# Kernel tuning notes

Measured on AMD Instinct MI355X. Metric: run time of the kernel, lower is better.

## Reference

```python
import jax, jax.numpy as jnp
import numpy as np

IMG = 640
SCORE_THR = 0.1
IOU_THR = 0.5
MAX_DET = 200  # fixed upper bound on kept boxes per class (jit-static)
BBOX_STD = (0.1, 0.1, 0.2, 0.2)  # standard RetinaNet delta std


def _make_anchors():
    # Standard RetinaNet anchors: P3-P7, 3 ratios x 3 scales, xyxy format.
    strides = [8, 16, 32, 64, 128]
    sizes = [32, 64, 128, 256, 512]
    ratios = np.array([0.5, 1.0, 2.0])
    scales = np.array([2 ** 0, 2 ** (1.0 / 3.0), 2 ** (2.0 / 3.0)])
    out = []
    for stride, size in zip(strides, sizes):
        n = IMG // stride
        ws = (size * scales[None, :] * np.sqrt(1.0 / ratios)[:, None]).reshape(-1)
        hs = (size * scales[None, :] * np.sqrt(ratios)[:, None]).reshape(-1)
        c = (np.arange(n) + 0.5) * stride
        CX, CY = np.meshgrid(c, c)
        ctr = np.stack([CX.ravel(), CY.ravel()], -1)  # [n*n, 2]
        wh = np.stack([ws, hs], -1)  # [9, 2]
        boxes = np.concatenate([ctr[:, None, :] - 0.5 * wh[None],
                                ctr[:, None, :] + 0.5 * wh[None]], -1)  # [n*n, 9, 4]
        out.append(boxes.reshape(-1, 4))
    return np.concatenate(out, 0).astype(np.float32)  # [76725, 4]


def setup_inputs() -> dict:
    key = jax.random.key(0)
    k1, k2 = jax.random.split(key)
    A = 76725
    C = 80
    classification = jax.random.uniform(k1, (1, A, C), dtype=jnp.float32)
    regression = jax.random.normal(k2, (1, A, 4), dtype=jnp.float32)
    anchors = jnp.asarray(_make_anchors())  # [A, 4] xyxy
    return {"classification": classification, "regression": regression, "anchors": anchors}


def _decode_and_clip(anchors, reg):
    aw = anchors[:, 2] - anchors[:, 0]
    ah = anchors[:, 3] - anchors[:, 1]
    ax = anchors[:, 0] + 0.5 * aw
    ay = anchors[:, 1] + 0.5 * ah
    cx = ax + reg[:, 0] * BBOX_STD[0] * aw
    cy = ay + reg[:, 1] * BBOX_STD[1] * ah
    w = aw * jnp.exp(reg[:, 2] * BBOX_STD[2])
    h = ah * jnp.exp(reg[:, 3] * BBOX_STD[3])
    x1 = jnp.clip(cx - 0.5 * w, 0.0, IMG)  # trimBox2Image
    y1 = jnp.clip(cy - 0.5 * h, 0.0, IMG)
    x2 = jnp.clip(cx + 0.5 * w, 0.0, IMG)
    y2 = jnp.clip(cy + 0.5 * h, 0.0, IMG)
    return jnp.stack([x1, y1, x2, y2], -1)  # [A, 4]


def reference(classification, regression, anchors):
    cls = classification[0]  # [A, C]
    boxes = _decode_and_clip(anchors, regression[0])  # [A, 4]
    A = cls.shape[0]
    C = cls.shape[1]
    idx = jnp.arange(A)
    areas = (boxes[:, 2] - boxes[:, 0]) * (boxes[:, 3] - boxes[:, 1])

    def nms_one(scores):  # scores: [A] for one class
        s0 = jnp.where(scores > SCORE_THR, scores, -1.0)
        keep0 = jnp.zeros((A,), dtype=bool)

        def step(carry, _):
            s, keep = carry
            i = jnp.argmax(s)
            valid = s[i] > 0.0
            keep = keep.at[i].set(valid)
            b = boxes[i]
            ix1 = jnp.maximum(b[0], boxes[:, 0])
            iy1 = jnp.maximum(b[1], boxes[:, 1])
            ix2 = jnp.minimum(b[2], boxes[:, 2])
            iy2 = jnp.minimum(b[3], boxes[:, 3])
            inter = jnp.clip(ix2 - ix1, 0.0) * jnp.clip(iy2 - iy1, 0.0)
            ab = (b[2] - b[0]) * (b[3] - b[1])
            iou = inter / (ab + areas - inter)
            sup = valid & ((iou > IOU_THR) | (idx == i))
            s = jnp.where(sup, -1.0, s)
            return (s, keep), None

        (_, keep), _ = jax.lax.scan(step, (s0, keep0), None, length=MAX_DET)
        return keep

    keep = jax.vmap(nms_one)(cls.T)  # [C, A] bool, greedy NMS per class
    final_scores = jnp.where(keep, cls.T, 0.0)  # [C, A]
    final_labels = jnp.where(keep, jnp.arange(C, dtype=jnp.int32)[:, None], -1)  # [C, A]
    final_boxes = jnp.where(keep[..., None], boxes[None], 0.0)  # [C, A, 4]
    return final_scores, final_labels, final_boxes, keep
```

## Files before the change

kernel.cpp:

```cpp
#include <hip/hip_runtime.h>
#include <cstdint>
#include <cstddef>

#pragma clang fp contract(off)

#define A_N 76725
#define C_N 80
#define CA_N (A_N * 80)
#define MAXDET 200
#define CAP 4096
#define NBIN 16
#define BCAP 256
#define IMG_F 640.0f
#define THR0 0.975f
#define CNT_STRIDE 32
#define FILLB 2480

typedef unsigned long long u64;

__device__ __forceinline__ bool iou_gt(float b0, float b1, float b2, float b3, float ab,
                                       float x0, float x1, float x2, float x3, float xa) {
    float ix1 = fmaxf(b0, x0);
    float iy1 = fmaxf(b1, x1);
    float ix2 = fminf(b2, x2);
    float iy2 = fminf(b3, x3);
    float iw = fmaxf(ix2 - ix1, 0.0f);
    float ih = fmaxf(iy2 - iy1, 0.0f);
    float inter = iw * ih;
    float den = ab + xa - inter;
    float iou = inter / den;
    return iou > 0.5f;
}

__device__ __forceinline__ float band_lo(int b) {
    return 0.975f - 0.025f * (float)b;
}

__global__ __launch_bounds__(256) void k_prep(const float* __restrict__ cls,
                                              const float* __restrict__ reg,
                                              const float* __restrict__ anc,
                                              float* __restrict__ boxes,
                                              int* __restrict__ gcnt,
                                              u64* __restrict__ gkeys) {
    int i = blockIdx.x * 256 + threadIdx.x;
    if (i < A_N) {
        float a0 = anc[i * 4 + 0], a1 = anc[i * 4 + 1];
        float a2 = anc[i * 4 + 2], a3 = anc[i * 4 + 3];
        float aw = a2 - a0;
        float ah = a3 - a1;
        float ax = a0 + 0.5f * aw;
        float ay = a1 + 0.5f * ah;
        float r0 = reg[i * 4 + 0], r1 = reg[i * 4 + 1];
        float r2 = reg[i * 4 + 2], r3 = reg[i * 4 + 3];
        float cx = ax + r0 * 0.1f * aw;
        float cy = ay + r1 * 0.1f * ah;
        float w = aw * expf(r2 * 0.2f);
        float h = ah * expf(r3 * 0.2f);
        float x1 = fminf(fmaxf(cx - 0.5f * w, 0.0f), IMG_F);
        float y1 = fminf(fmaxf(cy - 0.5f * h, 0.0f), IMG_F);
        float x2 = fminf(fmaxf(cx + 0.5f * w, 0.0f), IMG_F);
        float y2 = fminf(fmaxf(cy + 0.5f * h, 0.0f), IMG_F);
        boxes[i * 4 + 0] = x1;
        boxes[i * 4 + 1] = y1;
        boxes[i * 4 + 2] = x2;
        boxes[i * 4 + 3] = y2;
    }
    if (i < CA_N) {
        float s = cls[i];
        if (s > THR0) {
            int c = i % C_N;
            unsigned a = (unsigned)(i / C_N);
            int b = (int)((s - THR0) * 640.0f);
            b = b < 0 ? 0 : (b > (NBIN - 1) ? (NBIN - 1) : b);
            int slot = atomicAdd(&gcnt[(c * NBIN + b) * CNT_STRIDE], 1);
            if (slot < BCAP)
                gkeys[((size_t)(c * NBIN + b) << 8) + slot] =
                    ((u64)__float_as_uint(s) << 32) | (u64)(0xFFFFFFFFu - a);
        }
    }
}

__device__ __forceinline__ int resolve_run(const u64* seg, int cnt, int kept,
                                           const float4* __restrict__ boxes4,
                                           float4* kboxS, float* karea,
                                           int* kIdxL, float* kScrL,
                                           float4* cbxS, float* car,
                                           unsigned int* mlo, unsigned int* mhi,
                                           unsigned char* supp, int* keptL,
                                           int tid, int lane) {
    for (int cs = 0; cs < cnt && kept < MAXDET; cs += 64) {
        int nc = (cnt - cs < 64) ? (cnt - cs) : 64;
        float4 rb = make_float4(0.f, 0.f, 0.f, 0.f);
        float rar = 0.f, rsc = 0.f;
        int rix = 0;
        if (tid < 64) {
            mlo[tid] = 0;
            mhi[tid] = 0;
            supp[tid] = (tid < nc) ? 0 : 1;
            if (tid < nc) {
                u64 key = seg[cs + tid];
                rix = (int)(0xFFFFFFFFu - (unsigned)(key & 0xFFFFFFFFull));
                rsc = __uint_as_float((unsigned)(key >> 32));
                rb = boxes4[rix];
                rar = (rb.z - rb.x) * (rb.w - rb.y);
                cbxS[tid] = rb;
                car[tid] = rar;
            }
        }
        __syncthreads();

        {
            int i = tid >> 4, jl = tid & 15;
            if (i < nc) {
                float4 x = cbxS[i];
                float xa = car[i];
                bool s = false;
                for (int j = jl; j < kept; j += 16) {
                    float4 kb = kboxS[j];
                    if (iou_gt(kb.x, kb.y, kb.z, kb.w, karea[j],
                               x.x, x.y, x.z, x.w, xa)) { s = true; break; }
                }
                if (s) supp[i] = 1;
            }
        }
        {
            int i = tid & 63, jb = tid >> 6;
            if (i < nc) {
                float4 b = cbxS[i];
                float ba = car[i];
                unsigned int l32 = 0, h32 = 0;
                for (int j = jb; j < nc; j += 16) {
                    if (j > i) {
                        float4 o = cbxS[j];
                        if (iou_gt(b.x, b.y, b.z, b.w, ba,
                                   o.x, o.y, o.z, o.w, car[j])) {
                            if (j < 32) l32 |= 1u << j;
                            else        h32 |= 1u << (j - 32);
                        }
                    }
                }
                if (l32) atomicOr(&mlo[i], l32);
                if (h32) atomicOr(&mhi[i], h32);
            }
        }
        __syncthreads();

        if (tid < 64) {
            bool alive = (lane < nc) && (supp[lane] == 0);
            unsigned int myLo = mlo[lane], myHi = mhi[lane];
            int kc = kept;
            while (kc < MAXDET) {
                u64 av = __ballot(alive);
                if (av == 0ull) break;
                int i = (int)__builtin_ctzll(av);
                unsigned int plo = (unsigned)__shfl((int)myLo, i, 64);
                unsigned int phi = (unsigned)__shfl((int)myHi, i, 64);
                u64 mi = ((u64)phi << 32) | plo;
                if (lane == i) {
                    kboxS[kc] = rb;
                    karea[kc] = rar;
                    kIdxL[kc] = rix;
                    kScrL[kc] = rsc;
                    alive = false;
                }
                if ((mi >> lane) & 1ull) alive = false;
                kc++;
            }
            if (lane == 0) *keptL = kc;
        }
        __syncthreads();
        kept = *keptL;
    }
    return kept;
}

__global__ __launch_bounds__(1024) void k_mega(const float* __restrict__ cls,
                                               const float* __restrict__ boxes,
                                               const int* __restrict__ gcnt,
                                               const u64* __restrict__ gkeys,
                                               int* __restrict__ kcnt,
                                               int* __restrict__ kidx,
                                               float* __restrict__ kscr,
                                               float* __restrict__ kboxg,
                                               float4* __restrict__ out4) {
    const int tid = threadIdx.x;

    if (blockIdx.x >= C_N) {
        int fb = blockIdx.x - C_N;
        const int n4 = (7 * CA_N) / 4;
        const int lab_lo = CA_N / 4;
        const int lab_hi = (2 * CA_N) / 4;
        for (int i = fb * 1024 + tid; i < n4; i += FILLB * 1024) {
            float v = (i >= lab_lo && i < lab_hi) ? -1.0f : 0.0f;
            out4[i] = make_float4(v, v, v, v);
        }
        return;
    }

    const int c = blockIdx.x;
    const int wave = tid >> 6, lane = tid & 63;
    const float4* boxes4 = (const float4*)boxes;

    __shared__ u64 keys[CAP];
    __shared__ int bcnt[NBIN];
    __shared__ float4 kboxS[MAXDET];
    __shared__ float karea[MAXDET];
    __shared__ int kIdxL[MAXDET];
    __shared__ float kScrL[MAXDET];
    __shared__ float4 cbxS[64];
    __shared__ float car[64];
    __shared__ unsigned int mlo[64], mhi[64];
    __shared__ unsigned char supp[64];
    __shared__ int cntL, keptL;

    if (tid < NBIN) {
        int v = gcnt[(c * NBIN + tid) * CNT_STRIDE];
        bcnt[tid] = v > BCAP ? BCAP : v;
    }
    __syncthreads();

    {
        int cw = bcnt[wave];
        volatile u64* seg = keys + (wave << 8);
        const u64* src = gkeys + ((size_t)(c * NBIN + wave) << 8);
        for (int i = lane; i < cw; i += 64) seg[i] = src[i];
        int n2 = 64;
        while (n2 < cw) n2 <<= 1;
        for (int i = cw + lane; i < n2; i += 64) seg[i] = 0ull;
        __builtin_amdgcn_wave_barrier();
        for (int k = 2; k <= n2; k <<= 1) {
            for (int j = k >> 1; j > 0; j >>= 1) {
                for (int i0 = lane; i0 < n2; i0 += 64) {
                    int ixj = i0 ^ j;
                    if (ixj > i0) {
                        u64 u = seg[i0], v = seg[ixj];
                        bool up = ((i0 & k) == 0);
                        if (up ? (u < v) : (u > v)) { seg[i0] = v; seg[ixj] = u; }
                    }
                }
                __builtin_amdgcn_wave_barrier();
            }
        }
    }
    __syncthreads();

    int kept = 0;
    for (int b = NBIN - 1; b >= 0; --b) {
        kept = resolve_run(keys + (b << 8), bcnt[b], kept, boxes4,
                           kboxS, karea, kIdxL, kScrL, cbxS, car,
                           mlo, mhi, supp, &keptL, tid, lane);
        if (kept >= MAXDET) break;
    }

    if (kept < MAXDET) {
        for (int band = 1;; ++band) {
            float hiB = band_lo(band - 1);
            float lo = band_lo(band);
            bool last = (lo <= 0.1f);
            float loEff = last ? 0.1f : lo;
            if (tid == 0) cntL = 0;
            __syncthreads();
            for (int a = tid; a < A_N; a += 1024) {
                float s = cls[(size_t)a * C_N + c];
                if (s > loEff && s <= hiB) {
                    int p = atomicAdd(&cntL, 1);
                    if (p < CAP)
                        keys[p] = ((u64)__float_as_uint(s) << 32) |
                                  (u64)(0xFFFFFFFFu - (unsigned)a);
                }
            }
            __syncthreads();
            int cnt = cntL < CAP ? cntL : CAP;

            int n2 = 64;
            while (n2 < cnt) n2 <<= 1;
            for (int i = cnt + tid; i < n2; i += 1024) keys[i] = 0ull;
            __syncthreads();
            for (int k = 2; k <= n2; k <<= 1) {
                for (int j = k >> 1; j > 0; j >>= 1) {
                    for (int i = tid; i < n2; i += 1024) {
                        int ixj = i ^ j;
                        if (ixj > i) {
                            u64 u = keys[i], v = keys[ixj];
                            bool up = ((i & k) == 0);
                            if (up ? (u < v) : (u > v)) { keys[i] = v; keys[ixj] = u; }
                        }
                    }
                    __syncthreads();
                }
            }

            kept = resolve_run(keys, cnt, kept, boxes4,
                               kboxS, karea, kIdxL, kScrL, cbxS, car,
                               mlo, mhi, supp, &keptL, tid, lane);
            if (kept >= MAXDET || last) break;
        }
    }

    if (tid == 0) kcnt[c] = kept;
    for (int i = tid; i < kept; i += 1024) {
        kidx[c * MAXDET + i] = kIdxL[i];
        kscr[c * MAXDET + i] = kScrL[i];
        float4 kb = kboxS[i];
        kboxg[(c * MAXDET + i) * 4 + 0] = kb.x;
        kboxg[(c * MAXDET + i) * 4 + 1] = kb.y;
        kboxg[(c * MAXDET + i) * 4 + 2] = kb.z;
        kboxg[(c * MAXDET + i) * 4 + 3] = kb.w;
    }
}

__global__ __launch_bounds__(256) void k_scatter(const int* __restrict__ kcnt,
                                                 const int* __restrict__ kidx,
                                                 const float* __restrict__ kscr,
                                                 const float* __restrict__ kboxg,
                                                 float* __restrict__ out) {
    int c = blockIdx.x, t = threadIdx.x;
    int k = kcnt[c];
    for (int i = t; i < k; i += 256) {
        int a = kidx[c * MAXDET + i];
        size_t base = (size_t)c * A_N + (size_t)a;
        out[base] = kscr[c * MAXDET + i];
        out[(size_t)CA_N + base] = (float)c;
        size_t bo = (size_t)2 * CA_N + base * 4;
        out[bo + 0] = kboxg[(c * MAXDET + i) * 4 + 0];
        out[bo + 1] = kboxg[(c * MAXDET + i) * 4 + 1];
        out[bo + 2] = kboxg[(c * MAXDET + i) * 4 + 2];
        out[bo + 3] = kboxg[(c * MAXDET + i) * 4 + 3];
        out[(size_t)6 * CA_N + base] = 1.0f;
    }
}

extern "C" void kernel_launch(void* const* d_in, const int* in_sizes, int n_in,
                              void* d_out, int out_size, void* d_ws, size_t ws_size,
                              hipStream_t stream) {
    const float* cls = (const float*)d_in[0];
    const float* reg = (const float*)d_in[1];
    const float* anc = (const float*)d_in[2];
    float* out = (float*)d_out;

    int* gcnt = (int*)d_ws;
    float* boxes = (float*)(gcnt + C_N * NBIN * CNT_STRIDE);
    u64* gkeys = (u64*)(boxes + 4 * A_N);
    int* kcnt = (int*)(gkeys + (size_t)C_N * NBIN * BCAP);
    int* kidx = kcnt + C_N;
    float* kscr = (float*)(kidx + C_N * MAXDET);
    float* kboxg = kscr + C_N * MAXDET;

    hipMemsetAsync(gcnt, 0, C_N * NBIN * CNT_STRIDE * sizeof(int), stream);

    k_prep<<<(CA_N + 255) / 256, 256, 0, stream>>>(cls, reg, anc, boxes, gcnt, gkeys);

    k_mega<<<C_N + FILLB, 1024, 0, stream>>>(cls, boxes, gcnt, gkeys,
                                             kcnt, kidx, kscr, kboxg, (float4*)d_out);

    k_scatter<<<C_N, 256, 0, stream>>>(kcnt, kidx, kscr, kboxg, out);
}
```

Before: 276.1 us.

## Replace chunked NMS with bitmask-matrix NMS and split sort into separate kernel

The output zero-fill moves from extra blocks of the mega kernel into the prep kernel via a grid-stride loop. Per-class bin sorting moves into its own k_sort kernel. The resolve kernel takes the top up to 512 candidates in sorted order, builds a full 512x512 upper-triangular IoU suppression bitmask in shared memory, and resolves greedy NMS in one wave with readlane. Kept results are written straight to the output, which removes the separate scatter kernel and its staging buffers. The aim is to cut the serial 64-chunk resolve passes and their barriers, at the cost of an extra kernel launch and more shared memory per block.

```diff
diff --git a/kernel.cpp b/kernel.cpp
--- a/kernel.cpp
+++ b/kernel.cpp
@@ -8,13 +8,13 @@
 #define C_N 80
 #define CA_N (A_N * 80)
 #define MAXDET 200
-#define CAP 4096
 #define NBIN 16
 #define BCAP 256
+#define W_N 512
+#define WORDS 8
 #define IMG_F 640.0f
 #define THR0 0.975f
 #define CNT_STRIDE 32
-#define FILLB 2480
 
 typedef unsigned long long u64;
 
@@ -36,12 +36,20 @@
     return 0.975f - 0.025f * (float)b;
 }
 
+__device__ __forceinline__ u64 readlane64(u64 v, int src) {
+    unsigned lo = __builtin_amdgcn_readlane((unsigned)v, src);
+    unsigned hi = __builtin_amdgcn_readlane((unsigned)(v >> 32), src);
+    return ((u64)hi << 32) | lo;
+}
+
 __global__ __launch_bounds__(256) void k_prep(const float* __restrict__ cls,
                                               const float* __restrict__ reg,
                                               const float* __restrict__ anc,
                                               float* __restrict__ boxes,
                                               int* __restrict__ gcnt,
-                                              u64* __restrict__ gkeys) {
+                                              u64* __restrict__ gkeys,
+                                              float4* __restrict__ out4,
+                                              int nthreads) {
     int i = blockIdx.x * 256 + threadIdx.x;
     if (i < A_N) {
         float a0 = anc[i * 4 + 0], a1 = anc[i * 4 + 1];
@@ -78,12 +86,50 @@
                     ((u64)__float_as_uint(s) << 32) | (u64)(0xFFFFFFFFu - a);
         }
     }
+    const int n4 = (7 * CA_N) / 4;
+    const int lab_lo = CA_N / 4;
+    const int lab_hi = (2 * CA_N) / 4;
+    for (int q = i; q < n4; q += nthreads) {
+        float v = (q >= lab_lo && q < lab_hi) ? -1.0f : 0.0f;
+        out4[q] = make_float4(v, v, v, v);
+    }
+}
+
+__global__ __launch_bounds__(1024) void k_sort(const int* __restrict__ gcnt,
+                                               u64* __restrict__ gkeys) {
+    const int c = blockIdx.x;
+    const int wave = threadIdx.x >> 6, lane = threadIdx.x & 63;
+    __shared__ u64 buf[NBIN][BCAP];
+
+    int cnt = gcnt[(c * NBIN + wave) * CNT_STRIDE];
+    cnt = cnt > BCAP ? BCAP : cnt;
+    u64* gsrc = gkeys + ((size_t)(c * NBIN + wave) << 8);
+    volatile u64* seg = buf[wave];
+    for (int i = lane; i < cnt; i += 64) seg[i] = gsrc[i];
+    int n2 = 64;
+    while (n2 < cnt) n2 <<= 1;
+    for (int i = cnt + lane; i < n2; i += 64) seg[i] = 0ull;
+    __builtin_amdgcn_wave_barrier();
+    for (int k = 2; k <= n2; k <<= 1) {
+        for (int j = k >> 1; j > 0; j >>= 1) {
+            for (int i0 = lane; i0 < n2; i0 += 64) {
+                int ixj = i0 ^ j;
+                if (ixj > i0) {
+                    u64 u = seg[i0], v = seg[ixj];
+                    bool up = ((i0 & k) == 0);
+                    if (up ? (u < v) : (u > v)) { seg[i0] = v; seg[ixj] = u; }
+                }
+            }
+            __builtin_amdgcn_wave_barrier();
+        }
+    }
+    for (int i = lane; i < cnt; i += 64) gsrc[i] = seg[i];
 }
 
 __device__ __forceinline__ int resolve_run(const u64* seg, int cnt, int kept,
                                            const float4* __restrict__ boxes4,
+                                           float* __restrict__ out, int c,
                                            float4* kboxS, float* karea,
-                                           int* kIdxL, float* kScrL,
                                            float4* cbxS, float* car,
                                            unsigned int* mlo, unsigned int* mhi,
                                            unsigned char* supp, int* keptL,
@@ -108,7 +154,6 @@
             }
         }
         __syncthreads();
-
         {
             int i = tid >> 4, jl = tid & 15;
             if (i < nc) {
@@ -144,7 +189,6 @@
             }
         }
         __syncthreads();
-
         if (tid < 64) {
             bool alive = (lane < nc) && (supp[lane] == 0);
             unsigned int myLo = mlo[lane], myHi = mhi[lane];
@@ -159,8 +203,15 @@
                 if (lane == i) {
                     kboxS[kc] = rb;
                     karea[kc] = rar;
-                    kIdxL[kc] = rix;
-                    kScrL[kc] = rsc;
+                    size_t base = (size_t)c * A_N + (size_t)rix;
+                    out[base] = rsc;
+                    out[(size_t)CA_N + base] = (float)c;
+                    size_t bo = (size_t)2 * CA_N + base * 4;
+                    out[bo + 0] = rb.x;
+                    out[bo + 1] = rb.y;
+                    out[bo + 2] = rb.z;
+                    out[bo + 3] = rb.w;
+                    out[(size_t)6 * CA_N + base] = 1.0f;
                     alive = false;
                 }
                 if ((mi >> lane) & 1ull) alive = false;
@@ -174,85 +225,162 @@
     return kept;
 }
 
-__global__ __launch_bounds__(1024) void k_mega(const float* __restrict__ cls,
-                                               const float* __restrict__ boxes,
-                                               const int* __restrict__ gcnt,
-                                               const u64* __restrict__ gkeys,
-                                               int* __restrict__ kcnt,
-                                               int* __restrict__ kidx,
-                                               float* __restrict__ kscr,
-                                               float* __restrict__ kboxg,
-                                               float4* __restrict__ out4) {
+__global__ __launch_bounds__(1024) void k_resolve(const float* __restrict__ cls,
+                                                  const float* __restrict__ boxes,
+                                                  const int* __restrict__ gcnt,
+                                                  const u64* __restrict__ gkeys,
+                                                  float* __restrict__ out) {
+    const int c = blockIdx.x;
     const int tid = threadIdx.x;
-
-    if (blockIdx.x >= C_N) {
-        int fb = blockIdx.x - C_N;
-        const int n4 = (7 * CA_N) / 4;
-        const int lab_lo = CA_N / 4;
-        const int lab_hi = (2 * CA_N) / 4;
-        for (int i = fb * 1024 + tid; i < n4; i += FILLB * 1024) {
-            float v = (i >= lab_lo && i < lab_hi) ? -1.0f : 0.0f;
-            out4[i] = make_float4(v, v, v, v);
-        }
-        return;
-    }
-
-    const int c = blockIdx.x;
-    const int wave = tid >> 6, lane = tid & 63;
+    const int lane = tid & 63;
     const float4* boxes4 = (const float4*)boxes;
 
-    __shared__ u64 keys[CAP];
-    __shared__ int bcnt[NBIN];
+    __shared__ u64 maskL[W_N * WORDS];
+    __shared__ float4 cbx[W_N];
+    __shared__ float car[W_N];
+    __shared__ int cntb[NBIN], off[NBIN];
     __shared__ float4 kboxS[MAXDET];
     __shared__ float karea[MAXDET];
-    __shared__ int kIdxL[MAXDET];
-    __shared__ float kScrL[MAXDET];
     __shared__ float4 cbxS[64];
-    __shared__ float car[64];
+    __shared__ float car64[64];
     __shared__ unsigned int mlo[64], mhi[64];
     __shared__ unsigned char supp[64];
-    __shared__ int cntL, keptL;
+    __shared__ u64 keptwS[WORDS];
+    __shared__ int keptCtr, keptSh, cntL, keptL;
 
     if (tid < NBIN) {
         int v = gcnt[(c * NBIN + tid) * CNT_STRIDE];
-        bcnt[tid] = v > BCAP ? BCAP : v;
+        cntb[tid] = v > BCAP ? BCAP : v;
+    }
+    if (tid == 0) keptCtr = 0;
+    __syncthreads();
+    if (tid < NBIN) {
+        int s = 0;
+        for (int bb = NBIN - 1; bb > tid; --bb) s += cntb[bb];
+        off[tid] = s;
+    }
+    __syncthreads();
+    const int N = off[0] + cntb[0];
+    const int NW = N < W_N ? N : W_N;
+
+    int myA = 0;
+    float mySc = 0.f, myArea = 0.f;
+    float4 myBox = make_float4(0.f, 0.f, 0.f, 0.f);
+    if (tid < NW) {
+        int b = NBIN - 1;
+        for (; b >= 0; --b)
+            if (tid >= off[b] && tid < off[b] + cntb[b]) break;
+        u64 key = gkeys[((size_t)(c * NBIN + b) << 8) + (tid - off[b])];
+        myA = (int)(0xFFFFFFFFu - (unsigned)(key & 0xFFFFFFFFull));
+        mySc = __uint_as_float((unsigned)(key >> 32));
+        myBox = boxes4[myA];
+        myArea = (myBox.z - myBox.x) * (myBox.w - myBox.y);
+        cbx[tid] = myBox;
+        car[tid] = myArea;
     }
     __syncthreads();
 
     {
-        int cw = bcnt[wave];
-        volatile u64* seg = keys + (wave << 8);
-        const u64* src = gkeys + ((size_t)(c * NBIN + wave) << 8);
-        for (int i = lane; i < cw; i += 64) seg[i] = src[i];
-        int n2 = 64;
-        while (n2 < cw) n2 <<= 1;
-        for (int i = cw + lane; i < n2; i += 64) seg[i] = 0ull;
-        __builtin_amdgcn_wave_barrier();
-        for (int k = 2; k <= n2; k <<= 1) {
-            for (int j = k >> 1; j > 0; j >>= 1) {
-                for (int i0 = lane; i0 < n2; i0 += 64) {
-                    int ixj = i0 ^ j;
-                    if (ixj > i0) {
-                        u64 u = seg[i0], v = seg[ixj];
-                        bool up = ((i0 & k) == 0);
-                        if (up ? (u < v) : (u > v)) { seg[i0] = v; seg[ixj] = u; }
-                    }
-                }
-                __builtin_amdgcn_wave_barrier();
-            }
-        }
-    }
-    __syncthreads();
-
-    int kept = 0;
-    for (int b = NBIN - 1; b >= 0; --b) {
-        kept = resolve_run(keys + (b << 8), bcnt[b], kept, boxes4,
-                           kboxS, karea, kIdxL, kScrL, cbxS, car,
-                           mlo, mhi, supp, &keptL, tid, lane);
-        if (kept >= MAXDET) break;
+        int w = tid & 7, ig = tid >> 3;
+        int r0 = ig * 4;
+        int jbase = w * 64;
+        if (r0 < NW) {
+            if (jbase + 63 <= r0) {
+                for (int r = 0; r < 4; ++r)
+                    if (r0 + r < NW) maskL[(size_t)(r0 + r) * WORDS + w] = 0ull;
+            } else {
+                float4 b0 = cbx[r0];
+                float4 b1 = (r0 + 1 < NW) ? cbx[r0 + 1] : b0;
+                float4 b2 = (r0 + 2 < NW) ? cbx[r0 + 2] : b0;
+                float4 b3 = (r0 + 3 < NW) ? cbx[r0 + 3] : b0;
+                float a0 = car[r0];
+                float a1 = (r0 + 1 < NW) ? car[r0 + 1] : a0;
+                float a2 = (r0 + 2 < NW) ? car[r0 + 2] : a0;
+                float a3 = (r0 + 3 < NW) ? car[r0 + 3] : a0;
+                u64 m0 = 0, m1 = 0, m2 = 0, m3 = 0;
+                int jend = jbase + 64 < NW ? jbase + 64 : NW;
+                for (int j = jbase; j < jend; ++j) {
+                    float4 o = cbx[j];
+                    float oa = car[j];
+                    u64 bit = 1ull << (j - jbase);
+                    if (j > r0 && iou_gt(b0.x, b0.y, b0.z, b0.w, a0,
+                                         o.x, o.y, o.z, o.w, oa)) m0 |= bit;
+                    if (j > r0 + 1 && iou_gt(b1.x, b1.y, b1.z, b1.w, a1,
+                                             o.x, o.y, o.z, o.w, oa)) m1 |= bit;
+                    if (j > r0 + 2 && iou_gt(b2.x, b2.y, b2.z, b2.w, a2,
+                                             o.x, o.y, o.z, o.w, oa)) m2 |= bit;
+                    if (j > r0 + 3 && iou_gt(b3.x, b3.y, b3.z, b3.w, a3,
+                                             o.x, o.y, o.z, o.w, oa)) m3 |= bit;
+                }
+                maskL[(size_t)r0 * WORDS + w] = m0;
+                if (r0 + 1 < NW) maskL[(size_t)(r0 + 1) * WORDS + w] = m1;
+                if (r0 + 2 < NW) maskL[(size_t)(r0 + 2) * WORDS + w] = m2;
+                if (r0 + 3 < NW) maskL[(size_t)(r0 + 3) * WORDS + w] = m3;
+            }
+        }
+    }
+    __syncthreads();
+
+    if (tid < 64) {
+        u64 rem = 0, keptw = 0;
+        int kept = 0;
+        for (int w0 = 0; w0 < WORDS && kept < MAXDET; ++w0) {
+            int nb = NW - w0 * 64;
+            if (nb <= 0) break;
+            u64 valw = nb >= 64 ? ~0ull : ((1ull << nb) - 1ull);
+            u64 alive = ~readlane64(rem, w0) & valw;
+            while (alive && kept < MAXDET) {
+                int ii = (int)__builtin_ctzll(alive);
+                int i = w0 * 64 + ii;
+                u64 m = 0;
+                if (lane < WORDS) m = maskL[(size_t)i * WORDS + lane];
+                rem |= m;
+                if (lane == w0) keptw |= 1ull << ii;
+                kept++;
+                u64 mw0 = readlane64(m, w0);
+                alive &= ~(mw0 | (1ull << ii));
+            }
+        }
+        if (lane < WORDS) keptwS[lane] = keptw;
+        if (lane == 0) keptSh = kept;
+    }
+    __syncthreads();
+
+    if (tid < NW) {
+        if ((keptwS[tid >> 6] >> (tid & 63)) & 1ull) {
+            int slot = atomicAdd(&keptCtr, 1);
+            kboxS[slot] = myBox;
+            karea[slot] = myArea;
+            size_t base = (size_t)c * A_N + (size_t)myA;
+            out[base] = mySc;
+            out[(size_t)CA_N + base] = (float)c;
+            size_t bo = (size_t)2 * CA_N + base * 4;
+            out[bo + 0] = myBox.x;
+            out[bo + 1] = myBox.y;
+            out[bo + 2] = myBox.z;
+            out[bo + 3] = myBox.w;
+            out[(size_t)6 * CA_N + base] = 1.0f;
+        }
+    }
+    __syncthreads();
+    int kept = keptSh;
+
+    if (kept < MAXDET && N > NW) {
+        u64* keysF = maskL;
+        for (int t2 = NW + tid; t2 < N; t2 += 1024) {
+            int b = NBIN - 1;
+            for (; b >= 0; --b)
+                if (t2 >= off[b] && t2 < off[b] + cntb[b]) break;
+            keysF[t2 - NW] = gkeys[((size_t)(c * NBIN + b) << 8) + (t2 - off[b])];
+        }
+        __syncthreads();
+        kept = resolve_run(keysF, N - NW, kept, boxes4, out, c,
+                           kboxS, karea, cbxS, car64, mlo, mhi, supp, &keptL,
+                           tid, lane);
     }
 
     if (kept < MAXDET) {
+        u64* keysF = maskL;
         for (int band = 1;; ++band) {
             float hiB = band_lo(band - 1);
             float lo = band_lo(band);
@@ -264,69 +392,35 @@
                 float s = cls[(size_t)a * C_N + c];
                 if (s > loEff && s <= hiB) {
                     int p = atomicAdd(&cntL, 1);
-                    if (p < CAP)
-                        keys[p] = ((u64)__float_as_uint(s) << 32) |
-                                  (u64)(0xFFFFFFFFu - (unsigned)a);
+                    if (p < 4096)
+                        keysF[p] = ((u64)__float_as_uint(s) << 32) |
+                                   (u64)(0xFFFFFFFFu - (unsigned)a);
                 }
             }
             __syncthreads();
-            int cnt = cntL < CAP ? cntL : CAP;
-
+            int cnt = cntL < 4096 ? cntL : 4096;
             int n2 = 64;
             while (n2 < cnt) n2 <<= 1;
-            for (int i = cnt + tid; i < n2; i += 1024) keys[i] = 0ull;
+            for (int i = cnt + tid; i < n2; i += 1024) keysF[i] = 0ull;
             __syncthreads();
             for (int k = 2; k <= n2; k <<= 1) {
                 for (int j = k >> 1; j > 0; j >>= 1) {
                     for (int i = tid; i < n2; i += 1024) {
                         int ixj = i ^ j;
                         if (ixj > i) {
-                            u64 u = keys[i], v = keys[ixj];
+                            u64 u = keysF[i], v = keysF[ixj];
                             bool up = ((i & k) == 0);
-                            if (up ? (u < v) : (u > v)) { keys[i] = v; keys[ixj] = u; }
+                            if (up ? (u < v) : (u > v)) { keysF[i] = v; keysF[ixj] = u; }
                         }
                     }
                     __syncthreads();
                 }
             }
-
-            kept = resolve_run(keys, cnt, kept, boxes4,
-                               kboxS, karea, kIdxL, kScrL, cbxS, car,
-                               mlo, mhi, supp, &keptL, tid, lane);
+            kept = resolve_run(keysF, cnt, kept, boxes4, out, c,
+                               kboxS, karea, cbxS, car64, mlo, mhi, supp, &keptL,
+                               tid, lane);
             if (kept >= MAXDET || last) break;
         }
-    }
-
-    if (tid == 0) kcnt[c] = kept;
-    for (int i = tid; i < kept; i += 1024) {
-        kidx[c * MAXDET + i] = kIdxL[i];
-        kscr[c * MAXDET + i] = kScrL[i];
-        float4 kb = kboxS[i];
-        kboxg[(c * MAXDET + i) * 4 + 0] = kb.x;
-        kboxg[(c * MAXDET + i) * 4 + 1] = kb.y;
-        kboxg[(c * MAXDET + i) * 4 + 2] = kb.z;
-        kboxg[(c * MAXDET + i) * 4 + 3] = kb.w;
-    }
-}
-
-__global__ __launch_bounds__(256) void k_scatter(const int* __restrict__ kcnt,
-                                                 const int* __restrict__ kidx,
-                                                 const float* __restrict__ kscr,
-                                                 const float* __restrict__ kboxg,
-                                                 float* __restrict__ out) {
-    int c = blockIdx.x, t = threadIdx.x;
-    int k = kcnt[c];
-    for (int i = t; i < k; i += 256) {
-        int a = kidx[c * MAXDET + i];
-        size_t base = (size_t)c * A_N + (size_t)a;
-        out[base] = kscr[c * MAXDET + i];
-        out[(size_t)CA_N + base] = (float)c;
-        size_t bo = (size_t)2 * CA_N + base * 4;
-        out[bo + 0] = kboxg[(c * MAXDET + i) * 4 + 0];
-        out[bo + 1] = kboxg[(c * MAXDET + i) * 4 + 1];
-        out[bo + 2] = kboxg[(c * MAXDET + i) * 4 + 2];
-        out[bo + 3] = kboxg[(c * MAXDET + i) * 4 + 3];
-        out[(size_t)6 * CA_N + base] = 1.0f;
     }
 }
 
@@ -341,17 +435,14 @@
     int* gcnt = (int*)d_ws;
     float* boxes = (float*)(gcnt + C_N * NBIN * CNT_STRIDE);
     u64* gkeys = (u64*)(boxes + 4 * A_N);
-    int* kcnt = (int*)(gkeys + (size_t)C_N * NBIN * BCAP);
-    int* kidx = kcnt + C_N;
-    float* kscr = (float*)(kidx + C_N * MAXDET);
-    float* kboxg = kscr + C_N * MAXDET;
 
     hipMemsetAsync(gcnt, 0, C_N * NBIN * CNT_STRIDE * sizeof(int), stream);
 
-    k_prep<<<(CA_N + 255) / 256, 256, 0, stream>>>(cls, reg, anc, boxes, gcnt, gkeys);
-
-    k_mega<<<C_N + FILLB, 1024, 0, stream>>>(cls, boxes, gcnt, gkeys,
-                                             kcnt, kidx, kscr, kboxg, (float4*)d_out);
-
-    k_scatter<<<C_N, 256, 0, stream>>>(kcnt, kidx, kscr, kboxg, out);
-}
+    const int nblocks = (CA_N + 255) / 256;
+    k_prep<<<nblocks, 256, 0, stream>>>(cls, reg, anc, boxes, gcnt, gkeys,
+                                        (float4*)d_out, nblocks * 256);
+
+    k_sort<<<C_N, 1024, 0, stream>>>(gcnt, gkeys);
+
+    k_resolve<<<C_N, 1024, 0, stream>>>(cls, boxes, gcnt, gkeys, out);
+}
```

Result: slower. 319.8 us (+15.8%).

## Replace per-bin sequential NMS runs with batched bitmask IoU matrix and wave scan

Applied to the files above, without the earlier changes.

The top up to 320 sorted candidates per class are gathered from all score bins at once. Their full upper-triangular IoU>0.5 bitmask matrix is computed in parallel across the block, and greedy selection is then done by a single wave using readlane over 64-bit mask words. This removes the many block-wide syncs and repeated kept-vs-candidate passes of the old per-bin 64-wide resolve loop. The old path stays as a fallback when fewer than 200 boxes survive. The cost is extra LDS for the candidate and mask buffers, and kept boxes are now written in atomic order rather than score order.

```diff
diff --git a/kernel.cpp b/kernel.cpp
--- a/kernel.cpp
+++ b/kernel.cpp
@@ -8,9 +8,10 @@
 #define C_N 80
 #define CA_N (A_N * 80)
 #define MAXDET 200
-#define CAP 4096
 #define NBIN 16
 #define BCAP 256
+#define W_N 320
+#define WORDS 5
 #define IMG_F 640.0f
 #define THR0 0.975f
 #define CNT_STRIDE 32
@@ -34,6 +35,12 @@
 
 __device__ __forceinline__ float band_lo(int b) {
     return 0.975f - 0.025f * (float)b;
+}
+
+__device__ __forceinline__ u64 readlane64(u64 v, int src) {
+    unsigned lo = __builtin_amdgcn_readlane((unsigned)v, src);
+    unsigned hi = __builtin_amdgcn_readlane((unsigned)(v >> 32), src);
+    return ((u64)hi << 32) | lo;
 }
 
 __global__ __launch_bounds__(256) void k_prep(const float* __restrict__ cls,
@@ -84,7 +91,7 @@
                                            const float4* __restrict__ boxes4,
                                            float4* kboxS, float* karea,
                                            int* kIdxL, float* kScrL,
-                                           float4* cbxS, float* car,
+                                           float4* cbxS, float* car64,
                                            unsigned int* mlo, unsigned int* mhi,
                                            unsigned char* supp, int* keptL,
                                            int tid, int lane) {
@@ -104,16 +111,15 @@
                 rb = boxes4[rix];
                 rar = (rb.z - rb.x) * (rb.w - rb.y);
                 cbxS[tid] = rb;
-                car[tid] = rar;
+                car64[tid] = rar;
             }
         }
         __syncthreads();
-
         {
             int i = tid >> 4, jl = tid & 15;
             if (i < nc) {
                 float4 x = cbxS[i];
-                float xa = car[i];
+                float xa = car64[i];
                 bool s = false;
                 for (int j = jl; j < kept; j += 16) {
                     float4 kb = kboxS[j];
@@ -124,16 +130,16 @@
             }
         }
         {
-            int i = tid & 63, jb = tid >> 6;
+            int i = tid & 63, jb2 = tid >> 6;
             if (i < nc) {
                 float4 b = cbxS[i];
-                float ba = car[i];
+                float ba = car64[i];
                 unsigned int l32 = 0, h32 = 0;
-                for (int j = jb; j < nc; j += 16) {
+                for (int j = jb2; j < nc; j += 16) {
                     if (j > i) {
                         float4 o = cbxS[j];
                         if (iou_gt(b.x, b.y, b.z, b.w, ba,
-                                   o.x, o.y, o.z, o.w, car[j])) {
+                                   o.x, o.y, o.z, o.w, car64[j])) {
                             if (j < 32) l32 |= 1u << j;
                             else        h32 |= 1u << (j - 32);
                         }
@@ -144,7 +150,6 @@
             }
         }
         __syncthreads();
-
         if (tid < 64) {
             bool alive = (lane < nc) && (supp[lane] == 0);
             unsigned int myLo = mlo[lane], myHi = mhi[lane];
@@ -201,27 +206,42 @@
     const int wave = tid >> 6, lane = tid & 63;
     const float4* boxes4 = (const float4*)boxes;
 
-    __shared__ u64 keys[CAP];
-    __shared__ int bcnt[NBIN];
+    __shared__ u64 buf[NBIN][BCAP];
+    __shared__ u64 maskS[W_N * WORDS];
+    __shared__ float4 cbx[W_N];
+    __shared__ float car[W_N];
+    __shared__ float cscr[W_N];
+    __shared__ int cidx[W_N];
     __shared__ float4 kboxS[MAXDET];
     __shared__ float karea[MAXDET];
     __shared__ int kIdxL[MAXDET];
     __shared__ float kScrL[MAXDET];
     __shared__ float4 cbxS[64];
-    __shared__ float car[64];
+    __shared__ float car64[64];
     __shared__ unsigned int mlo[64], mhi[64];
     __shared__ unsigned char supp[64];
-    __shared__ int cntL, keptL;
+    __shared__ int cntb[NBIN], off[NBIN];
+    __shared__ u64 kmS[WORDS];
+    __shared__ int keptShv, keptCtr, cntL, keptL;
 
     if (tid < NBIN) {
         int v = gcnt[(c * NBIN + tid) * CNT_STRIDE];
-        bcnt[tid] = v > BCAP ? BCAP : v;
-    }
-    __syncthreads();
+        cntb[tid] = v > BCAP ? BCAP : v;
+    }
+    if (tid == 0) keptCtr = 0;
+    __syncthreads();
+    if (tid < NBIN) {
+        int s = 0;
+        for (int bb = NBIN - 1; bb > tid; --bb) s += cntb[bb];
+        off[tid] = s;
+    }
+    __syncthreads();
+    const int N = off[0] + cntb[0];
+    const int NW = N < W_N ? N : W_N;
 
     {
-        int cw = bcnt[wave];
-        volatile u64* seg = keys + (wave << 8);
+        int cw = cntb[wave];
+        volatile u64* seg = buf[wave];
         const u64* src = gkeys + ((size_t)(c * NBIN + wave) << 8);
         for (int i = lane; i < cw; i += 64) seg[i] = src[i];
         int n2 = 64;
@@ -244,15 +264,114 @@
     }
     __syncthreads();
 
-    int kept = 0;
-    for (int b = NBIN - 1; b >= 0; --b) {
-        kept = resolve_run(keys + (b << 8), bcnt[b], kept, boxes4,
-                           kboxS, karea, kIdxL, kScrL, cbxS, car,
-                           mlo, mhi, supp, &keptL, tid, lane);
-        if (kept >= MAXDET) break;
+    for (int i = tid; i < NW; i += 1024) {
+        int b = NBIN - 1;
+        for (; b >= 0; --b)
+            if (i >= off[b] && i < off[b] + cntb[b]) break;
+        u64 key = buf[b][i - off[b]];
+        int a = (int)(0xFFFFFFFFu - (unsigned)(key & 0xFFFFFFFFull));
+        float4 bx = boxes4[a];
+        cbx[i] = bx;
+        car[i] = (bx.z - bx.x) * (bx.w - bx.y);
+        cscr[i] = __uint_as_float((unsigned)(key >> 32));
+        cidx[i] = a;
+    }
+    __syncthreads();
+
+    for (int idx = tid; idx < W_N * WORDS; idx += 1024) {
+        int r = idx / WORDS, w = idx - r * WORDS;
+        u64 m = 0;
+        if (r < NW) {
+            int jbase = w * 64;
+            int jend = (NW - jbase) < 64 ? (NW - jbase) : 64;
+            if (jend > 0 && jbase + 63 > r) {
+                float4 rb = cbx[r];
+                float ra = car[r];
+                for (int jj = 0; jj < jend; ++jj) {
+                    int jg = jbase + jj;
+                    if (jg > r) {
+                        float4 o = cbx[jg];
+                        if (iou_gt(rb.x, rb.y, rb.z, rb.w, ra,
+                                   o.x, o.y, o.z, o.w, car[jg]))
+                            m |= 1ull << jj;
+                    }
+                }
+            }
+        }
+        maskS[idx] = m;
+    }
+    __syncthreads();
+
+    if (tid < 64) {
+        int kept = 0;
+        u64 rem0 = 0, rem1 = 0, rem2 = 0, rem3 = 0, rem4 = 0;
+        u64 km0 = 0, km1 = 0, km2 = 0, km3 = 0, km4 = 0;
+
+#define SCAN_CHUNK(W0)                                                        \
+        if (W0 * 64 < NW && kept < MAXDET) {                                  \
+            int r = W0 * 64 + lane;                                           \
+            u64 r0 = maskS[r * WORDS + 0];                                    \
+            u64 r1 = maskS[r * WORDS + 1];                                    \
+            u64 r2 = maskS[r * WORDS + 2];                                    \
+            u64 r3 = maskS[r * WORDS + 3];                                    \
+            u64 r4 = maskS[r * WORDS + 4];                                    \
+            int nb = NW - W0 * 64;                                            \
+            u64 valw = nb >= 64 ? ~0ull : ((1ull << nb) - 1ull);              \
+            u64 alive = ~rem##W0 & valw;                                      \
+            while (alive && kept < MAXDET) {                                  \
+                int ii = (int)__builtin_ctzll(alive);                         \
+                u64 q0 = readlane64(r0, ii);                                  \
+                u64 q1 = readlane64(r1, ii);                                  \
+                u64 q2 = readlane64(r2, ii);                                  \
+                u64 q3 = readlane64(r3, ii);                                  \
+                u64 q4 = readlane64(r4, ii);                                  \
+                rem0 |= q0; rem1 |= q1; rem2 |= q2; rem3 |= q3; rem4 |= q4;   \
+                km##W0 |= 1ull << ii;                                         \
+                kept++;                                                       \
+                alive &= ~(q##W0 | (1ull << ii));                             \
+            }                                                                 \
+        }
+
+        SCAN_CHUNK(0)
+        SCAN_CHUNK(1)
+        SCAN_CHUNK(2)
+        SCAN_CHUNK(3)
+        SCAN_CHUNK(4)
+#undef SCAN_CHUNK
+
+        if (lane == 0) {
+            kmS[0] = km0; kmS[1] = km1; kmS[2] = km2; kmS[3] = km3; kmS[4] = km4;
+            keptShv = kept;
+        }
+    }
+    __syncthreads();
+
+    for (int i = tid; i < NW; i += 1024) {
+        if ((kmS[i >> 6] >> (i & 63)) & 1ull) {
+            int slot = atomicAdd(&keptCtr, 1);
+            kboxS[slot] = cbx[i];
+            karea[slot] = car[i];
+            kIdxL[slot] = cidx[i];
+            kScrL[slot] = cscr[i];
+        }
+    }
+    __syncthreads();
+    int kept = keptShv;
+
+    if (kept < MAXDET && N > NW) {
+        for (int b = NBIN - 1; b >= 0 && kept < MAXDET; --b) {
+            int s0 = off[b], sz = cntb[b];
+            int start = NW > s0 ? (NW - s0) : 0;
+            if (start < sz)
+                kept = resolve_run((const u64*)buf[b] + start, sz - start, kept,
+                                   boxes4, kboxS, karea, kIdxL, kScrL,
+                                   cbxS, car64, mlo, mhi, supp, &keptL,
+                                   tid, lane);
+        }
     }
 
     if (kept < MAXDET) {
+        u64* keysF = &buf[0][0];
         for (int band = 1;; ++band) {
             float hiB = band_lo(band - 1);
             float lo = band_lo(band);
@@ -264,35 +383,33 @@
                 float s = cls[(size_t)a * C_N + c];
                 if (s > loEff && s <= hiB) {
                     int p = atomicAdd(&cntL, 1);
-                    if (p < CAP)
-                        keys[p] = ((u64)__float_as_uint(s) << 32) |
-                                  (u64)(0xFFFFFFFFu - (unsigned)a);
+                    if (p < 4096)
+                        keysF[p] = ((u64)__float_as_uint(s) << 32) |
+                                   (u64)(0xFFFFFFFFu - (unsigned)a);
                 }
             }
             __syncthreads();
-            int cnt = cntL < CAP ? cntL : CAP;
-
+            int cnt = cntL < 4096 ? cntL : 4096;
             int n2 = 64;
             while (n2 < cnt) n2 <<= 1;
-            for (int i = cnt + tid; i < n2; i += 1024) keys[i] = 0ull;
+            for (int i = cnt + tid; i < n2; i += 1024) keysF[i] = 0ull;
             __syncthreads();
             for (int k = 2; k <= n2; k <<= 1) {
                 for (int j = k >> 1; j > 0; j >>= 1) {
                     for (int i = tid; i < n2; i += 1024) {
                         int ixj = i ^ j;
                         if (ixj > i) {
-                            u64 u = keys[i], v = keys[ixj];
+                            u64 u = keysF[i], v = keysF[ixj];
                             bool up = ((i & k) == 0);
-                            if (up ? (u < v) : (u > v)) { keys[i] = v; keys[ixj] = u; }
+                            if (up ? (u < v) : (u > v)) { keysF[i] = v; keysF[ixj] = u; }
                         }
                     }
                     __syncthreads();
                 }
             }
-
-            kept = resolve_run(keys, cnt, kept, boxes4,
-                               kboxS, karea, kIdxL, kScrL, cbxS, car,
-                               mlo, mhi, supp, &keptL, tid, lane);
+            kept = resolve_run(keysF, cnt, kept, boxes4,
+                               kboxS, karea, kIdxL, kScrL,
+                               cbxS, car64, mlo, mhi, supp, &keptL, tid, lane);
             if (kept >= MAXDET || last) break;
         }
     }
```

New measurement: 270.6 us. 2.0% less time.
